# Kernel tuning notes

Hardware: AMD Instinct MI355X
Metric: run time of the kernel (lower is better)

## Reference

```python
import jax, jax.numpy as jnp
import numpy as np

B, S, E, H = 4, 2048, 1024, 16
D = E // H


def setup_inputs() -> dict:
    key = jax.random.key(0)
    ks = jax.random.split(key, 8)
    inv = 1.0 / np.sqrt(E)
    return {
        "query": jax.random.normal(ks[0], (B, S, E), dtype=jnp.float32),
        "key": jax.random.normal(ks[1], (B, S, E), dtype=jnp.float32),
        "value": jax.random.normal(ks[2], (B, S, E), dtype=jnp.float32),
        "key_padding_mask": jnp.zeros((B, S), dtype=bool),
        "Wq": jax.random.uniform(ks[3], (E, E), jnp.float32, -inv, inv),
        "Wk": jax.random.uniform(ks[4], (E, E), jnp.float32, -inv, inv),
        "Wv": jax.random.uniform(ks[5], (E, E), jnp.float32, -inv, inv),
        "Wo": jax.random.uniform(ks[6], (E, E), jnp.float32, -inv, inv),
        "gamma": jnp.ones((H,), dtype=jnp.float32),
    }


def reference(query, key, value, key_padding_mask, Wq, Wk, Wv, Wo, gamma):
    b, s, e = query.shape
    h = gamma.shape[0]
    d = e // h
    # torch Linear: x @ W.T ; split into heads -> [b, h, s, d]
    q = (query @ Wq.T).reshape(b, s, h, d).swapaxes(1, 2)
    k = (key @ Wk.T).reshape(b, key.shape[1], h, d).swapaxes(1, 2)
    v = (value @ Wv.T).reshape(b, value.shape[1], h, d).swapaxes(1, 2)
    scores = jnp.einsum("bhqd,bhkd->bhqk", q, k) / jnp.sqrt(jnp.asarray(d, q.dtype))
    scores = jnp.where(key_padding_mask[:, None, None, :], -jnp.inf, scores)
    attn = jax.nn.softmax(scores, axis=-1)  # dropout p=0 in eval-equivalent reference
    out = jnp.einsum("bhqk,bhkd->bhqd", attn, v)
    out = out * gamma[None, :, None, None]  # head-scale
    out = out.swapaxes(1, 2).reshape(b, s, e)
    return out @ Wo.T
```

## Files before the change

kernel.cpp:

```cpp
#include <hip/hip_runtime.h>
#include <hip/hip_bf16.h>
#include <cstdint>

typedef __bf16 bf16;
typedef __bf16 bf16_8 __attribute__((ext_vector_type(8)));
typedef __bf16 bf16_4 __attribute__((ext_vector_type(4)));
typedef float f32_4 __attribute__((ext_vector_type(4)));
typedef short s16x4 __attribute__((ext_vector_type(4)));
typedef short s16x8 __attribute__((ext_vector_type(8)));

#define MFMA_16x16x32(a, b, c) __builtin_amdgcn_mfma_f32_16x16x32_bf16((a), (b), (c), 0, 0, 0)

__device__ __forceinline__ void gll16(const void* g, void* l) {
  __builtin_amdgcn_global_load_lds((const __attribute__((address_space(1))) void*)g,
                                   (__attribute__((address_space(3))) void*)l, 16, 0, 0);
}

__device__ __forceinline__ float exp2fast(float x) {
#if __has_builtin(__builtin_amdgcn_exp2f)
  return __builtin_amdgcn_exp2f(x);
#else
  return __exp2f(x);
#endif
}

__device__ __forceinline__ unsigned bfbits(float x) {
  bf16 b = (bf16)x;
  return (unsigned)__builtin_bit_cast(unsigned short, b);
}

__global__ __launch_bounds__(256) void cvt_all(const float* __restrict__ q,
                                               const float* __restrict__ k,
                                               const float* __restrict__ v,
                                               const float* __restrict__ w0,
                                               const float* __restrict__ w1,
                                               const float* __restrict__ w2,
                                               const float* __restrict__ w3,
                                               bf16* __restrict__ qb,
                                               bf16* __restrict__ kb,
                                               bf16* __restrict__ vb,
                                               bf16* __restrict__ wb) {
  const int y = blockIdx.y;
  if (y < 3) {
    const float* src = y == 0 ? q : (y == 1 ? k : v);
    bf16* dst = y == 0 ? qb : (y == 1 ? kb : vb);
    size_t i = ((size_t)blockIdx.x * 256 + threadIdx.x) * 8;
    float4 f0 = *(const float4*)(src + i);
    float4 f1 = *(const float4*)(src + i + 4);
    bf16_8 o;
    o[0] = (bf16)f0.x; o[1] = (bf16)f0.y; o[2] = (bf16)f0.z; o[3] = (bf16)f0.w;
    o[4] = (bf16)f1.x; o[5] = (bf16)f1.y; o[6] = (bf16)f1.z; o[7] = (bf16)f1.w;
    *(bf16_8*)(dst + i) = o;
  } else {
    size_t i = ((size_t)blockIdx.x * 256 + threadIdx.x) * 4;
    const int widx = (int)(i >> 20);
    const size_t off = i & (((size_t)1 << 20) - 1);
    const float* srcs[4] = {w0, w1, w2, w3};
    const float sc = (widx == 0) ? 0.18033688f : 1.0f;
    float4 f = *(const float4*)(srcs[widx] + off);
    bf16_4 o;
    o[0] = (bf16)(f.x * sc); o[1] = (bf16)(f.y * sc);
    o[2] = (bf16)(f.z * sc); o[3] = (bf16)(f.w * sc);
    *(bf16_4*)(wb + i) = o;
  }
}

__global__ __launch_bounds__(256) void gemm_qkv(const bf16* __restrict__ Aq,
                                                const bf16* __restrict__ Ak,
                                                const bf16* __restrict__ Av,
                                                const bf16* __restrict__ W,
                                                bf16* __restrict__ Qp,
                                                bf16* __restrict__ Kp,
                                                bf16* __restrict__ Vt) {
  constexpr int BM = 128, BK = 32, K = 1024, N = 1024, M_S = 2048;
  __shared__ alignas(16) bf16 As[2][BM * BK];
  __shared__ alignas(16) bf16 Bs[2][BM * BK];

  const int tid = threadIdx.x;
  const int wave = tid >> 6, lane = tid & 63;
  const int quad = lane >> 4, l15 = lane & 15;
  const int wm = (wave & 1) * 64, wn = (wave >> 1) * 64;
  const int tensor = blockIdx.y >> 3;
  const int n0 = (blockIdx.y & 7) * 128;
  const size_t m0 = (size_t)blockIdx.x * BM;

  const bf16* A = tensor == 0 ? Aq : (tensor == 1 ? Ak : Av);
  const bf16* Bt = W + ((size_t)tensor << 20);

  f32_4 acc[4][4] = {};

  const size_t g_laneoff = (size_t)(lane >> 2) * K + (lane & 3) * 8;
  const bf16* Ag = A + (m0 + wave * 32) * (size_t)K + g_laneoff;
  const bf16* Bg = Bt + ((size_t)n0 + wave * 32) * (size_t)K + g_laneoff;
  const int l_off = wave * 32 * BK + lane * 8;

  auto stage = [&](int b, int k0) {
    gll16(Ag + k0, &As[b][l_off]);
    gll16(Ag + 16 * (size_t)K + k0, &As[b][l_off + 16 * BK]);
    gll16(Bg + k0, &Bs[b][l_off]);
    gll16(Bg + 16 * (size_t)K + k0, &Bs[b][l_off + 16 * BK]);
  };

  stage(0, 0);
  int buf = 0;
  for (int k0 = 0; k0 < K; k0 += BK, buf ^= 1) {
    __syncthreads();
    if (k0 + BK < K) stage(buf ^ 1, k0 + BK);

    bf16_8 af[4], bfr[4];
#pragma unroll
    for (int mt = 0; mt < 4; ++mt)
      af[mt] = *(const bf16_8*)&As[buf][(wm + mt * 16 + l15) * BK + quad * 8];
#pragma unroll
    for (int nt = 0; nt < 4; ++nt)
      bfr[nt] = *(const bf16_8*)&Bs[buf][(wn + nt * 16 + l15) * BK + quad * 8];
#pragma unroll
    for (int mt = 0; mt < 4; ++mt)
#pragma unroll
      for (int nt = 0; nt < 4; ++nt)
        acc[mt][nt] = MFMA_16x16x32(af[mt], bfr[nt], acc[mt][nt]);
  }

  if (tensor < 2) {
    bf16* C = tensor == 0 ? Qp : Kp;
#pragma unroll
    for (int mt = 0; mt < 4; ++mt)
#pragma unroll
      for (int i = 0; i < 4; ++i) {
        size_t row = m0 + wm + mt * 16 + quad * 4 + i;
        bf16* cr = C + row * N + n0 + wn + l15;
#pragma unroll
        for (int nt = 0; nt < 4; ++nt) cr[nt * 16] = (bf16)acc[mt][nt][i];
      }
  } else {
    const int bb = (int)(m0 >> 11);
    const int sbase = (int)(m0 & 2047) + wm;
#pragma unroll
    for (int mt = 0; mt < 4; ++mt)
#pragma unroll
      for (int nt = 0; nt < 4; ++nt) {
        int col = n0 + wn + nt * 16 + l15;
        bf16_4 pk;
        pk[0] = (bf16)acc[mt][nt][0]; pk[1] = (bf16)acc[mt][nt][1];
        pk[2] = (bf16)acc[mt][nt][2]; pk[3] = (bf16)acc[mt][nt][3];
        bf16* dst = Vt + ((size_t)(bb * 16 + (col >> 6)) * 64 + (col & 63)) * M_S +
                    sbase + (mt >> 1) * 32 + quad * 8 + (mt & 1) * 4;
        *(bf16_4*)dst = pk;
      }
  }
}

__global__ __launch_bounds__(256) void gemm_out(const bf16* __restrict__ A,
                                                const bf16* __restrict__ Bt,
                                                float* __restrict__ C,
                                                int M, int N, int K) {
  constexpr int BM = 128, BN = 128, BK = 32;
  __shared__ alignas(16) bf16 As[2][BM * BK];
  __shared__ alignas(16) bf16 Bs[2][BN * BK];

  const int tid = threadIdx.x;
  const int wave = tid >> 6, lane = tid & 63;
  const int quad = lane >> 4, l15 = lane & 15;
  const int wm = (wave & 1) * 64, wn = (wave >> 1) * 64;
  const size_t m0 = (size_t)blockIdx.x * BM;
  const size_t n0 = (size_t)blockIdx.y * BN;

  f32_4 acc[4][4] = {};

  const size_t g_laneoff = (size_t)(lane >> 2) * K + (lane & 3) * 8;
  const bf16* Ag = A + (m0 + wave * 32) * (size_t)K + g_laneoff;
  const bf16* Bg = Bt + (n0 + wave * 32) * (size_t)K + g_laneoff;
  const int l_off = wave * 32 * BK + lane * 8;

  auto stage = [&](int b, int k0) {
    gll16(Ag + k0, &As[b][l_off]);
    gll16(Ag + 16 * (size_t)K + k0, &As[b][l_off + 16 * BK]);
    gll16(Bg + k0, &Bs[b][l_off]);
    gll16(Bg + 16 * (size_t)K + k0, &Bs[b][l_off + 16 * BK]);
  };

  stage(0, 0);
  int buf = 0;
  for (int k0 = 0; k0 < K; k0 += BK, buf ^= 1) {
    __syncthreads();
    if (k0 + BK < K) stage(buf ^ 1, k0 + BK);

    bf16_8 af[4], bfr[4];
#pragma unroll
    for (int mt = 0; mt < 4; ++mt)
      af[mt] = *(const bf16_8*)&As[buf][(wm + mt * 16 + l15) * BK + quad * 8];
#pragma unroll
    for (int nt = 0; nt < 4; ++nt)
      bfr[nt] = *(const bf16_8*)&Bs[buf][(wn + nt * 16 + l15) * BK + quad * 8];
#pragma unroll
    for (int mt = 0; mt < 4; ++mt)
#pragma unroll
      for (int nt = 0; nt < 4; ++nt)
        acc[mt][nt] = MFMA_16x16x32(af[mt], bfr[nt], acc[mt][nt]);
  }

#pragma unroll
  for (int mt = 0; mt < 4; ++mt)
#pragma unroll
    for (int i = 0; i < 4; ++i) {
      size_t row = m0 + wm + mt * 16 + quad * 4 + i;
      float* cr = C + row * N + n0 + wn + l15;
#pragma unroll
      for (int nt = 0; nt < 4; ++nt) cr[nt * 16] = acc[mt][nt][i];
    }
}

__global__ __launch_bounds__(256, 4) void attn_fused(const bf16* __restrict__ Q,
                                                     const bf16* __restrict__ K,
                                                     const bf16* __restrict__ Vt,
                                                     const unsigned char* __restrict__ mask,
                                                     const float* __restrict__ gamma,
                                                     bf16* __restrict__ Out) {
  constexpr int S = 2048, E = 1024;
  constexpr float NEGB = -3.0e38f;
  __shared__ alignas(16) bf16 Ks[2][64 * 64];
  __shared__ alignas(16) bf16 Vs[2][64 * 64];

  const int tid = threadIdx.x;
  const int wave = tid >> 6, lane = tid & 63;
  const int quad = lane >> 4, l15 = lane & 15;

  const int bx = blockIdx.x, by = blockIdx.y;
  const int wx = (bx >> 3) | ((by & 7) << 1);
  const int bh = (bx & 7) | (by & ~7);
  const int q0 = wx * 128;
  const int b = bh >> 4, h = bh & 15;

  const unsigned char* mg = mask + (size_t)b * S;

  bool anym;
  {
    const uint4* m4 = (const uint4*)mg;
    uint4 x = m4[lane * 2], y = m4[lane * 2 + 1];
    unsigned o = (x.x | x.y | x.z | x.w) | (y.x | y.y | y.z | y.w);
    anym = __ballot(o != 0) != 0ull;
  }

  const int lrow = lane >> 3;
  const int sx = ((lane & 7) ^ lrow) * 8;
  const size_t koff = (size_t)lrow * E + sx;
  const size_t voff = (size_t)lrow * S + sx;

  const bf16* Qg = Q + ((size_t)(b * S + q0)) * E + h * 64;
  const bf16* Kg = K + ((size_t)b * S) * E + h * 64;
  const bf16* Vg = Vt + ((size_t)bh * 64) * S;

  auto stageKV = [&](int bf_, int kt) {
#pragma unroll
    for (int p = 0; p < 2; ++p) {
      gll16(Kg + (size_t)(kt + wave * 16 + p * 8) * E + koff,
            &Ks[bf_][(wave * 16 + p * 8) * 64 + lane * 8]);
      gll16(Vg + (size_t)(wave * 16 + p * 8) * S + voff + kt,
            &Vs[bf_][(wave * 16 + p * 8) * 64 + lane * 8]);
    }
  };

  stageKV(0, 0);

  bf16_8 qf[2][2];
#pragma unroll
  for (int mt = 0; mt < 2; ++mt)
#pragma unroll
    for (int ks = 0; ks < 2; ++ks)
      qf[mt][ks] = *(const bf16_8*)(Qg + (size_t)(wave * 32 + mt * 16 + l15) * E +
                                    ks * 32 + quad * 8);

  s16x8 onesP;
#pragma unroll
  for (int j = 0; j < 8; ++j) onesP[j] = (short)0x3F80;
  const bf16_8 onesA8 = __builtin_bit_cast(bf16_8, onesP);

  f32_4 accO[4][2] = {};
  f32_4 accR[2] = {};

  int buf = 0;
  for (int kt = 0; kt < S; kt += 64, buf ^= 1) {
    __syncthreads();
    if (kt + 64 < S) stageKV(buf ^ 1, kt + 64);

    f32_4 sT[4][2] = {};
    __builtin_amdgcn_s_setprio(1);
#pragma unroll
    for (int ks = 0; ks < 2; ++ks)
#pragma unroll
      for (int t = 0; t < 4; ++t) {
        bf16_8 af = *(const bf16_8*)&Ks[buf][(t * 16 + l15) * 64 +
                                            (((ks * 4 + quad) ^ (l15 & 7)) * 8)];
        sT[t][0] = MFMA_16x16x32(af, qf[0][ks], sT[t][0]);
        sT[t][1] = MFMA_16x16x32(af, qf[1][ks], sT[t][1]);
      }
    __builtin_amdgcn_s_setprio(0);

    s16x4 pk[4][2];
#pragma unroll
    for (int t = 0; t < 4; ++t) {
      float bb0 = 0.0f, bb1 = 0.0f, bb2 = 0.0f, bb3 = 0.0f;
      if (anym) {
        const unsigned um = *(const unsigned*)(mg + kt + t * 16 + quad * 4);
        bb0 = (um & 0xffu) ? NEGB : 0.0f;
        bb1 = (um & 0xff00u) ? NEGB : 0.0f;
        bb2 = (um & 0xff0000u) ? NEGB : 0.0f;
        bb3 = (um & 0xff000000u) ? NEGB : 0.0f;
      }
#pragma unroll
      for (int mt = 0; mt < 2; ++mt) {
        float e0 = exp2fast(sT[t][mt][0] + bb0);
        float e1 = exp2fast(sT[t][mt][1] + bb1);
        float e2 = exp2fast(sT[t][mt][2] + bb2);
        float e3 = exp2fast(sT[t][mt][3] + bb3);
        uint2 u;
        u.x = bfbits(e0) | (bfbits(e1) << 16);
        u.y = bfbits(e2) | (bfbits(e3) << 16);
        pk[t][mt] = __builtin_bit_cast(s16x4, u);
      }
    }

    __builtin_amdgcn_s_setprio(1);
#pragma unroll
    for (int i2 = 0; i2 < 2; ++i2) {
      const bf16_8 pb0 = __builtin_bit_cast(bf16_8,
          __builtin_shufflevector(pk[2 * i2][0], pk[2 * i2 + 1][0], 0, 1, 2, 3, 4, 5, 6, 7));
      const bf16_8 pb1 = __builtin_bit_cast(bf16_8,
          __builtin_shufflevector(pk[2 * i2][1], pk[2 * i2 + 1][1], 0, 1, 2, 3, 4, 5, 6, 7));
      accR[0] = MFMA_16x16x32(onesA8, pb0, accR[0]);
      accR[1] = MFMA_16x16x32(onesA8, pb1, accR[1]);
      const int xo = ((i2 * 4 + quad) ^ (l15 & 7)) * 8;
#pragma unroll
      for (int dt = 0; dt < 4; ++dt) {
        bf16_8 vf = *(const bf16_8*)&Vs[buf][(dt * 16 + l15) * 64 + xo];
        accO[dt][0] = MFMA_16x16x32(vf, pb0, accO[dt][0]);
        accO[dt][1] = MFMA_16x16x32(vf, pb1, accO[dt][1]);
      }
    }
    __builtin_amdgcn_s_setprio(0);
  }

  const float g = gamma[h];
  float invv[2];
#pragma unroll
  for (int mt = 0; mt < 2; ++mt) invv[mt] = g / accR[mt][0];

#pragma unroll
  for (int mt = 0; mt < 2; ++mt) {
    size_t token = (size_t)(b * S) + q0 + wave * 32 + mt * 16 + l15;
    bf16* orow = Out + token * E + h * 64;
#pragma unroll
    for (int dt = 0; dt < 4; ++dt) {
      bf16_4 ov;
      ov[0] = (bf16)(accO[dt][mt][0] * invv[mt]);
      ov[1] = (bf16)(accO[dt][mt][1] * invv[mt]);
      ov[2] = (bf16)(accO[dt][mt][2] * invv[mt]);
      ov[3] = (bf16)(accO[dt][mt][3] * invv[mt]);
      *(bf16_4*)(orow + dt * 16 + quad * 4) = ov;
    }
  }
}

extern "C" void kernel_launch(void* const* d_in, const int* in_sizes, int n_in,
                              void* d_out, int out_size, void* d_ws, size_t ws_size,
                              hipStream_t stream) {
  constexpr int Bb = 4, S = 2048, E = 1024;
  constexpr int M = Bb * S;

  const float* q = (const float*)d_in[0];
  const float* k = (const float*)d_in[1];
  const float* v = (const float*)d_in[2];
  const unsigned char* mask = (const unsigned char*)d_in[3];
  const float* Wq = (const float*)d_in[4];
  const float* Wk = (const float*)d_in[5];
  const float* Wv = (const float*)d_in[6];
  const float* Wo = (const float*)d_in[7];
  const float* gamma = (const float*)d_in[8];

  char* ws = (char*)d_ws;
  bf16* Wb = (bf16*)ws;
  bf16* qb = (bf16*)(ws + ((size_t)8 << 20));
  bf16* kb = (bf16*)(ws + ((size_t)24 << 20));
  bf16* vb = (bf16*)(ws + ((size_t)40 << 20));
  bf16* Vt = (bf16*)(ws + ((size_t)56 << 20));
  bf16* Qp = (bf16*)d_out;
  bf16* Kp = (bf16*)d_out + ((size_t)1 << 23);

  cvt_all<<<dim3(4096, 4), 256, 0, stream>>>(q, k, v, Wq, Wk, Wv, Wo, qb, kb, vb, Wb);

  gemm_qkv<<<dim3(M / 128, 24), 256, 0, stream>>>(qb, kb, vb, Wb, Qp, Kp, Vt);

  bf16* At = qb;
  attn_fused<<<dim3(S / 128, Bb * 16), 256, 0, stream>>>(Qp, Kp, Vt, mask, gamma, At);

  gemm_out<<<dim3(M / 128, E / 128), 256, 0, stream>>>(At, Wb + (3 << 20), (float*)d_out, M, E, E);
}
```

Measured before the change: 337.8 us.

## Fuse fp32-to-bf16 activation conversion into QKV GEMM A-tile loads

Drops the separate pass that converted query/key/value activations to bf16. The QKV GEMM now loads fp32 A tiles into LDS through an XOR-swizzled layout and converts them to bf16 in registers just before the MFMA. This removes a full write and re-read of the bf16 activation copies. In exchange, each A tile moves twice as many bytes from global memory into LDS, uses more LDS, and the conversion is repeated for each of the 8 N-column tiles.

After: 351.0 us. +3.9%, slower.

```diff
diff --git a/kernel.cpp b/kernel.cpp
--- a/kernel.cpp
+++ b/kernel.cpp
@@ -29,51 +29,39 @@
   return (unsigned)__builtin_bit_cast(unsigned short, b);
 }
 
-__global__ __launch_bounds__(256) void cvt_all(const float* __restrict__ q,
-                                               const float* __restrict__ k,
-                                               const float* __restrict__ v,
-                                               const float* __restrict__ w0,
-                                               const float* __restrict__ w1,
-                                               const float* __restrict__ w2,
-                                               const float* __restrict__ w3,
-                                               bf16* __restrict__ qb,
-                                               bf16* __restrict__ kb,
-                                               bf16* __restrict__ vb,
-                                               bf16* __restrict__ wb) {
-  const int y = blockIdx.y;
-  if (y < 3) {
-    const float* src = y == 0 ? q : (y == 1 ? k : v);
-    bf16* dst = y == 0 ? qb : (y == 1 ? kb : vb);
-    size_t i = ((size_t)blockIdx.x * 256 + threadIdx.x) * 8;
-    float4 f0 = *(const float4*)(src + i);
-    float4 f1 = *(const float4*)(src + i + 4);
-    bf16_8 o;
-    o[0] = (bf16)f0.x; o[1] = (bf16)f0.y; o[2] = (bf16)f0.z; o[3] = (bf16)f0.w;
-    o[4] = (bf16)f1.x; o[5] = (bf16)f1.y; o[6] = (bf16)f1.z; o[7] = (bf16)f1.w;
-    *(bf16_8*)(dst + i) = o;
-  } else {
-    size_t i = ((size_t)blockIdx.x * 256 + threadIdx.x) * 4;
-    const int widx = (int)(i >> 20);
-    const size_t off = i & (((size_t)1 << 20) - 1);
-    const float* srcs[4] = {w0, w1, w2, w3};
-    const float sc = (widx == 0) ? 0.18033688f : 1.0f;
-    float4 f = *(const float4*)(srcs[widx] + off);
-    bf16_4 o;
-    o[0] = (bf16)(f.x * sc); o[1] = (bf16)(f.y * sc);
-    o[2] = (bf16)(f.z * sc); o[3] = (bf16)(f.w * sc);
-    *(bf16_4*)(wb + i) = o;
-  }
-}
-
-__global__ __launch_bounds__(256) void gemm_qkv(const bf16* __restrict__ Aq,
-                                                const bf16* __restrict__ Ak,
-                                                const bf16* __restrict__ Av,
+__device__ __forceinline__ bf16_8 cvt8(float4 a, float4 b) {
+  bf16_8 v;
+  v[0] = (bf16)a.x; v[1] = (bf16)a.y; v[2] = (bf16)a.z; v[3] = (bf16)a.w;
+  v[4] = (bf16)b.x; v[5] = (bf16)b.y; v[6] = (bf16)b.z; v[7] = (bf16)b.w;
+  return v;
+}
+
+__global__ __launch_bounds__(256) void cvt_w(const float* __restrict__ w0,
+                                             const float* __restrict__ w1,
+                                             const float* __restrict__ w2,
+                                             const float* __restrict__ w3,
+                                             bf16* __restrict__ wb) {
+  size_t i = ((size_t)blockIdx.x * 256 + threadIdx.x) * 4;
+  const int widx = (int)(i >> 20);
+  const size_t off = i & (((size_t)1 << 20) - 1);
+  const float* srcs[4] = {w0, w1, w2, w3};
+  const float sc = (widx == 0) ? 0.18033688f : 1.0f;
+  float4 f = *(const float4*)(srcs[widx] + off);
+  bf16_4 o;
+  o[0] = (bf16)(f.x * sc); o[1] = (bf16)(f.y * sc);
+  o[2] = (bf16)(f.z * sc); o[3] = (bf16)(f.w * sc);
+  *(bf16_4*)(wb + i) = o;
+}
+
+__global__ __launch_bounds__(256) void gemm_qkv(const float* __restrict__ Aq,
+                                                const float* __restrict__ Ak,
+                                                const float* __restrict__ Av,
                                                 const bf16* __restrict__ W,
                                                 bf16* __restrict__ Qp,
                                                 bf16* __restrict__ Kp,
                                                 bf16* __restrict__ Vt) {
   constexpr int BM = 128, BK = 32, K = 1024, N = 1024, M_S = 2048;
-  __shared__ alignas(16) bf16 As[2][BM * BK];
+  __shared__ alignas(16) float Asf[2][BM * BK];
   __shared__ alignas(16) bf16 Bs[2][BM * BK];
 
   const int tid = threadIdx.x;
@@ -84,33 +72,43 @@
   const int n0 = (blockIdx.y & 7) * 128;
   const size_t m0 = (size_t)blockIdx.x * BM;
 
-  const bf16* A = tensor == 0 ? Aq : (tensor == 1 ? Ak : Av);
+  const float* A = tensor == 0 ? Aq : (tensor == 1 ? Ak : Av);
   const bf16* Bt = W + ((size_t)tensor << 20);
 
   f32_4 acc[4][4] = {};
 
+  const int lrow8 = lane >> 3;
+  const int lchk = (lane & 7) ^ lrow8;
+  const float* Agf = A + (m0 + wave * 32 + lrow8) * (size_t)K + lchk * 4;
+  const int adst = (wave * 32) * BK + lane * 4;
+
   const size_t g_laneoff = (size_t)(lane >> 2) * K + (lane & 3) * 8;
-  const bf16* Ag = A + (m0 + wave * 32) * (size_t)K + g_laneoff;
   const bf16* Bg = Bt + ((size_t)n0 + wave * 32) * (size_t)K + g_laneoff;
   const int l_off = wave * 32 * BK + lane * 8;
 
   auto stage = [&](int b, int k0) {
-    gll16(Ag + k0, &As[b][l_off]);
-    gll16(Ag + 16 * (size_t)K + k0, &As[b][l_off + 16 * BK]);
+#pragma unroll
+    for (int p = 0; p < 4; ++p)
+      gll16(Agf + (size_t)(p * 8) * K + k0, &Asf[b][adst + p * 8 * BK]);
     gll16(Bg + k0, &Bs[b][l_off]);
     gll16(Bg + 16 * (size_t)K + k0, &Bs[b][l_off + 16 * BK]);
   };
 
   stage(0, 0);
   int buf = 0;
+  const int r = l15 & 7;
   for (int k0 = 0; k0 < K; k0 += BK, buf ^= 1) {
     __syncthreads();
     if (k0 + BK < K) stage(buf ^ 1, k0 + BK);
 
     bf16_8 af[4], bfr[4];
 #pragma unroll
-    for (int mt = 0; mt < 4; ++mt)
-      af[mt] = *(const bf16_8*)&As[buf][(wm + mt * 16 + l15) * BK + quad * 8];
+    for (int mt = 0; mt < 4; ++mt) {
+      const float* rp = &Asf[buf][(wm + mt * 16 + l15) * BK];
+      float4 A0 = *(const float4*)(rp + ((2 * quad) ^ r) * 4);
+      float4 A1 = *(const float4*)(rp + ((2 * quad + 1) ^ r) * 4);
+      af[mt] = cvt8(A0, A1);
+    }
 #pragma unroll
     for (int nt = 0; nt < 4; ++nt)
       bfr[nt] = *(const bf16_8*)&Bs[buf][(wn + nt * 16 + l15) * BK + quad * 8];
@@ -379,18 +377,15 @@
 
   char* ws = (char*)d_ws;
   bf16* Wb = (bf16*)ws;
-  bf16* qb = (bf16*)(ws + ((size_t)8 << 20));
-  bf16* kb = (bf16*)(ws + ((size_t)24 << 20));
-  bf16* vb = (bf16*)(ws + ((size_t)40 << 20));
+  bf16* At = (bf16*)(ws + ((size_t)8 << 20));
   bf16* Vt = (bf16*)(ws + ((size_t)56 << 20));
   bf16* Qp = (bf16*)d_out;
   bf16* Kp = (bf16*)d_out + ((size_t)1 << 23);
 
-  cvt_all<<<dim3(4096, 4), 256, 0, stream>>>(q, k, v, Wq, Wk, Wv, Wo, qb, kb, vb, Wb);
-
-  gemm_qkv<<<dim3(M / 128, 24), 256, 0, stream>>>(qb, kb, vb, Wb, Qp, Kp, Vt);
-
-  bf16* At = qb;
+  cvt_w<<<dim3(4096), 256, 0, stream>>>(Wq, Wk, Wv, Wo, Wb);
+
+  gemm_qkv<<<dim3(M / 128, 24), 256, 0, stream>>>(q, k, v, Wb, Qp, Kp, Vt);
+
   attn_fused<<<dim3(S / 128, Bb * 16), 256, 0, stream>>>(Qp, Kp, Vt, mask, gamma, At);
 
   gemm_out<<<dim3(M / 128, E / 128), 256, 0, stream>>>(At, Wb + (3 << 20), (float*)d_out, M, E, E);
```
